# Optimization experiments

Measured on AMD Instinct MI355X. Metric: run time of the kernel, lower is better.

Reference implementation:

```python
import jax, jax.numpy as jnp
import numpy as np

EMBED_DIM = 1024
NUM_HEADS = 16
HEAD_DIM = EMBED_DIM // NUM_HEADS
B, T = 2, 2048


def setup_inputs() -> dict:
    key = jax.random.key(0)
    ks = jax.random.split(key, 9)
    s = 1.0 / np.sqrt(EMBED_DIM)
    x = jax.random.normal(ks[0], (B, T, EMBED_DIM), dtype=jnp.float32)
    Wq = jax.random.uniform(ks[1], (EMBED_DIM, EMBED_DIM), jnp.float32, -s, s)
    bq = jax.random.uniform(ks[2], (EMBED_DIM,), jnp.float32, -s, s)
    Wk = jax.random.uniform(ks[3], (EMBED_DIM, EMBED_DIM), jnp.float32, -s, s)
    bk = jax.random.uniform(ks[4], (EMBED_DIM,), jnp.float32, -s, s)
    Wv = jax.random.uniform(ks[5], (EMBED_DIM, EMBED_DIM), jnp.float32, -s, s)
    bv = jax.random.uniform(ks[6], (EMBED_DIM,), jnp.float32, -s, s)
    Wo = jax.random.uniform(ks[7], (EMBED_DIM, EMBED_DIM), jnp.float32, -s, s)
    bo = jax.random.uniform(ks[8], (EMBED_DIM,), jnp.float32, -s, s)
    return {"x": x, "Wq": Wq, "bq": bq, "Wk": Wk, "bk": bk,
            "Wv": Wv, "bv": bv, "Wo": Wo, "bo": bo}


def reference(x, Wq, bq, Wk, bk, Wv, bv, Wo, bo):
    Bx, Tx, D = x.shape
    # projections (torch Linear: y = x @ W^T + b); here W stored as [in, out]
    q = (x @ Wq + bq).reshape(Bx, Tx, NUM_HEADS, HEAD_DIM).transpose(0, 2, 1, 3)
    k = (x @ Wk + bk).reshape(Bx, Tx, NUM_HEADS, HEAD_DIM).transpose(0, 2, 1, 3)
    v = (x @ Wv + bv).reshape(Bx, Tx, NUM_HEADS, HEAD_DIM).transpose(0, 2, 1, 3)
    scale = HEAD_DIM ** -0.5
    attn = jnp.einsum('bhqd,bhkd->bhqk', q, k) * scale  # [B, H, T, T]
    causal = jnp.tril(jnp.ones((Tx, Tx), dtype=bool))
    attn = jnp.where(causal[None, None], attn, -jnp.inf)
    attn = jax.nn.softmax(attn, axis=-1)
    out = jnp.einsum('bhqk,bhkd->bhqd', attn, v)  # [B, H, T, hd]
    out = out.transpose(0, 2, 1, 3).reshape(Bx, Tx, D)
    return out @ Wo + bo
```

## Files before the change

kernel.cpp:

```cpp
#include <hip/hip_runtime.h>

#define EMBED 1024
#define NHEADS 16
#define HDIM 64
#define SEQ 2048
#define BATCH 2
#define MROWS (BATCH * SEQ)

using bf16x8 = __attribute__((ext_vector_type(8))) short;
using f32x4  = __attribute__((ext_vector_type(4))) float;
using us4    = __attribute__((ext_vector_type(4))) unsigned short;
using u32x2  = __attribute__((ext_vector_type(2))) unsigned int;

__device__ __forceinline__ unsigned short f2bf(float f) {
    unsigned int u = __builtin_bit_cast(unsigned int, f);
    u = (u + 0x7fffu + ((u >> 16) & 1u)) >> 16;
    return (unsigned short)u;
}

__device__ __forceinline__ unsigned int cvt_pk_bf16(float a, float b) {
    unsigned int d;
    asm("v_cvt_pk_bf16_f32 %0, %1, %2" : "=v"(d) : "v"(a), "v"(b));
    return d;
}

__device__ __forceinline__ void async16(const unsigned short* g, unsigned short* l) {
    __builtin_amdgcn_global_load_lds(
        (const __attribute__((address_space(1))) void*)g,
        (__attribute__((address_space(3))) void*)l, 16, 0, 0);
}

__global__ __launch_bounds__(256)
void cvt_all(const float* __restrict__ X, unsigned short* __restrict__ XO,
             const float* __restrict__ W0, const float* __restrict__ W1,
             const float* __restrict__ W2, const float* __restrict__ W3,
             unsigned short* __restrict__ T0, unsigned short* __restrict__ T1,
             unsigned short* __restrict__ T2, unsigned short* __restrict__ T3)
{
    const int tid = threadIdx.x;
    if (blockIdx.z == 4) {
        const int blk = blockIdx.y * 16 + blockIdx.x;
#pragma unroll
        for (int it = 0; it < 16; ++it) {
            int i = (blk * 16 + it) * 256 + tid;
            float4 v = ((const float4*)X)[i];
            us4 o;
            o[0] = f2bf(v.x); o[1] = f2bf(v.y); o[2] = f2bf(v.z); o[3] = f2bf(v.w);
            ((us4*)XO)[i] = o;
        }
        return;
    }
    const float* W = blockIdx.z == 0 ? W0 : blockIdx.z == 1 ? W1 :
                     blockIdx.z == 2 ? W2 : W3;
    unsigned short* T = blockIdx.z == 0 ? T0 : blockIdx.z == 1 ? T1 :
                        blockIdx.z == 2 ? T2 : T3;
    __shared__ unsigned short tile[64][72];
    const int k0 = blockIdx.y << 6, n0 = blockIdx.x << 6;
    const int lr = tid >> 4, lc = (tid & 15) << 2;
#pragma unroll
    for (int it = 0; it < 4; ++it) {
        int kr = lr + it * 16;
        float4 v = *(const float4*)(W + (size_t)(k0 + kr) * EMBED + n0 + lc);
        tile[lc + 0][kr] = f2bf(v.x);
        tile[lc + 1][kr] = f2bf(v.y);
        tile[lc + 2][kr] = f2bf(v.z);
        tile[lc + 3][kr] = f2bf(v.w);
    }
    __syncthreads();
#pragma unroll
    for (int it = 0; it < 4; ++it) {
        int nr = lr + it * 16;
        us4 o = *(const us4*)(&tile[nr][lc]);
        *(us4*)(T + (size_t)(n0 + nr) * EMBED + k0 + lc) = o;
    }
}

__device__ __forceinline__ void mfma_gemm_core(
    const unsigned short* __restrict__ A, const unsigned short* __restrict__ Bt,
    int bm, int n0, unsigned short* As, unsigned short* Bs,
    int wv, int lane, f32x4 acc[4][4])
{
    const int m16 = lane & 15, quad = lane >> 4;
    const int mb = (wv >> 1) << 6;
    const int nb = (wv & 1) << 6;
    const int rsw = m16 & 3;

    const int srow0 = lane >> 2;
    const int gcol  = ((lane & 3) ^ (srow0 & 3)) << 3;
    const unsigned short* ga = A  + (size_t)(bm + wv * 16 + srow0) * EMBED + gcol;
    const unsigned short* gb = Bt + (size_t)(n0 + wv * 16 + srow0) * EMBED + gcol;

    int offA[4], offB[4];
#pragma unroll
    for (int i = 0; i < 4; ++i) {
        offA[i] = (mb + i * 16 + m16) * 32;
        offB[i] = (nb + i * 16 + m16) * 32;
    }

    const int NK = EMBED / 32;
#define STAGE(t) do {                                                        \
        unsigned short* la = As + ((t) & 1) * (128 * 32) + wv * 16 * 32;     \
        unsigned short* lb = Bs + ((t) & 1) * (128 * 32) + wv * 16 * 32;     \
        const unsigned short* gat = ga + (t) * 32;                           \
        const unsigned short* gbt = gb + (t) * 32;                           \
        async16(gat, la);                                                    \
        async16(gat + 64 * EMBED, la + 64 * 32);                             \
        async16(gbt, lb);                                                    \
        async16(gbt + 64 * EMBED, lb + 64 * 32);                             \
    } while (0)

    STAGE(0);
    for (int t = 0; t < NK; ++t) {
        if (t + 1 < NK) {
            STAGE(t + 1);
            asm volatile("s_waitcnt vmcnt(4)" ::: "memory");
        } else {
            asm volatile("s_waitcnt vmcnt(0)" ::: "memory");
        }
        asm volatile("s_barrier" ::: "memory");
        const unsigned short* Ab = As + (t & 1) * (128 * 32);
        const unsigned short* Bb = Bs + (t & 1) * (128 * 32);
        const int sl = ((quad ^ rsw) << 3);
        bf16x8 af[4], bfv[4];
#pragma unroll
        for (int i = 0; i < 4; ++i) {
            af[i]  = *(const bf16x8*)(Ab + offA[i] + sl);
            bfv[i] = *(const bf16x8*)(Bb + offB[i] + sl);
        }
#pragma unroll
        for (int i = 0; i < 4; ++i)
#pragma unroll
            for (int j = 0; j < 4; ++j)
                acc[i][j] = __builtin_amdgcn_mfma_f32_16x16x32_bf16(
                    af[i], bfv[j], acc[i][j], 0, 0, 0);
        asm volatile("s_barrier" ::: "memory");
    }
#undef STAGE
}

__device__ __forceinline__ void mfma_gemm_core64(
    const unsigned short* __restrict__ A, const unsigned short* __restrict__ Bt,
    int bm, int n0, unsigned short* As, unsigned short* Bs,
    int wv, int lane, f32x4 acc[4][2])
{
    const int m16 = lane & 15, quad = lane >> 4;
    const int mb = (wv >> 1) << 6;
    const int nb = (wv & 1) << 5;
    const int rsw = m16 & 7;

    const int gcol = ((lane & 7) ^ ((lane >> 3) & 7)) << 3;
    const unsigned short* ga = A  + (size_t)(bm + wv * 32 + (lane >> 3)) * EMBED + gcol;
    const unsigned short* gb = Bt + (size_t)(n0 + wv * 16 + (lane >> 3)) * EMBED + gcol;

    int offA[4], offB[2];
#pragma unroll
    for (int i = 0; i < 4; ++i) offA[i] = (mb + i * 16 + m16) * 64;
#pragma unroll
    for (int j = 0; j < 2; ++j) offB[j] = (nb + j * 16 + m16) * 64;

    const int NK = EMBED / 64;
#define STAGE64(t) do {                                                      \
        unsigned short* la = As + ((t) & 1) * (128 * 64) + wv * 32 * 64;     \
        unsigned short* lb = Bs + ((t) & 1) * (64 * 64) + wv * 16 * 64;      \
        const unsigned short* gat = ga + (t) * 64;                           \
        const unsigned short* gbt = gb + (t) * 64;                           \
        _Pragma("unroll")                                                    \
        for (int j = 0; j < 4; ++j)                                          \
            async16(gat + j * 8 * EMBED, la + j * 8 * 64);                   \
        _Pragma("unroll")                                                    \
        for (int j = 0; j < 2; ++j)                                          \
            async16(gbt + j * 8 * EMBED, lb + j * 8 * 64);                   \
    } while (0)

    STAGE64(0);
    for (int t = 0; t < NK; ++t) {
        if (t + 1 < NK) {
            STAGE64(t + 1);
            asm volatile("s_waitcnt vmcnt(6)" ::: "memory");
        } else {
            asm volatile("s_waitcnt vmcnt(0)" ::: "memory");
        }
        asm volatile("s_barrier" ::: "memory");
        const unsigned short* Ab = As + (t & 1) * (128 * 64);
        const unsigned short* Bb = Bs + (t & 1) * (64 * 64);
#pragma unroll
        for (int ks = 0; ks < 2; ++ks) {
            const int sl = (((ks << 2) + quad) ^ rsw) << 3;
            bf16x8 af[4], bfv[2];
#pragma unroll
            for (int i = 0; i < 4; ++i)
                af[i] = *(const bf16x8*)(Ab + offA[i] + sl);
#pragma unroll
            for (int j = 0; j < 2; ++j)
                bfv[j] = *(const bf16x8*)(Bb + offB[j] + sl);
#pragma unroll
            for (int i = 0; i < 4; ++i)
#pragma unroll
                for (int j = 0; j < 2; ++j)
                    acc[i][j] = __builtin_amdgcn_mfma_f32_16x16x32_bf16(
                        af[i], bfv[j], acc[i][j], 0, 0, 0);
        }
        asm volatile("s_barrier" ::: "memory");
    }
#undef STAGE64
}

__global__ __launch_bounds__(256)
void qkv_gemm(const unsigned short* __restrict__ xb,
              const unsigned short* __restrict__ Wtq,
              const unsigned short* __restrict__ Wtk,
              const unsigned short* __restrict__ Wtv,
              const float* __restrict__ bq, const float* __restrict__ bk,
              const float* __restrict__ bv,
              unsigned short* __restrict__ Qo, unsigned short* __restrict__ Ko,
              unsigned short* __restrict__ Vto)
{
    __shared__ __align__(16) unsigned short As[2 * 128 * 32];
    __shared__ __align__(16) unsigned short Bs[2 * 128 * 32];
    const int tid = threadIdx.x, wv = tid >> 6, lane = tid & 63;
    const int m16 = lane & 15, quad = lane >> 4;
    const int which = blockIdx.x >> 3;
    const int n0 = (blockIdx.x & 7) << 7;
    const int bm = blockIdx.y << 7;
    const unsigned short* Bt = which == 0 ? Wtq : which == 1 ? Wtk : Wtv;
    const float* bias = which == 0 ? bq : which == 1 ? bk : bv;

    f32x4 acc[4][4];
#pragma unroll
    for (int i = 0; i < 4; ++i)
#pragma unroll
        for (int j = 0; j < 4; ++j) acc[i][j] = (f32x4){0.f, 0.f, 0.f, 0.f};

    mfma_gemm_core(xb, Bt, bm, n0, As, Bs, wv, lane, acc);

    const int mb = (wv >> 1) << 6, nb = (wv & 1) << 6;
    const float qscale = 0.125f * 1.4426950408889634f;
#pragma unroll
    for (int i = 0; i < 4; ++i) {
        const int m0 = bm + mb + i * 16 + quad * 4;
        const int b = m0 >> 11, t0 = m0 & (SEQ - 1);
#pragma unroll
        for (int j = 0; j < 4; ++j) {
            const int n = n0 + nb + j * 16 + m16;
            const int h = n >> 6, d = n & 63;
            const float bval = bias[n];
            if (which == 2) {
                us4 v;
#pragma unroll
                for (int r = 0; r < 4; ++r) v[r] = f2bf(acc[i][j][r] + bval);
                *(us4*)(Vto + ((((size_t)(b * NHEADS + h)) << 6) + d) * SEQ + t0) = v;
            } else {
                const float sc = which == 0 ? qscale : 1.f;
                unsigned short* dst = (which == 0 ? Qo : Ko) +
                    ((((size_t)(b * NHEADS + h)) << 11) + t0) * 64 + d;
#pragma unroll
                for (int r = 0; r < 4; ++r)
                    dst[(size_t)r * 64] = f2bf((acc[i][j][r] + bval) * sc);
            }
        }
    }
}

__global__ __launch_bounds__(256)
void out_gemm(const unsigned short* __restrict__ aob,
              const unsigned short* __restrict__ Wto,
              const float* __restrict__ bo, float* __restrict__ out)
{
    __shared__ __align__(16) unsigned short As[2 * 128 * 64];
    __shared__ __align__(16) unsigned short Bs[2 * 64 * 64];
    const int tid = threadIdx.x, wv = tid >> 6, lane = tid & 63;
    const int m16 = lane & 15, quad = lane >> 4;
    const int n0 = blockIdx.x << 6;
    const int bm = blockIdx.y << 7;

    f32x4 acc[4][2];
#pragma unroll
    for (int i = 0; i < 4; ++i)
#pragma unroll
        for (int j = 0; j < 2; ++j) acc[i][j] = (f32x4){0.f, 0.f, 0.f, 0.f};

    mfma_gemm_core64(aob, Wto, bm, n0, As, Bs, wv, lane, acc);

    const int mb = (wv >> 1) << 6, nb = (wv & 1) << 5;
#pragma unroll
    for (int i = 0; i < 4; ++i) {
        const int m0 = bm + mb + i * 16 + quad * 4;
#pragma unroll
        for (int j = 0; j < 2; ++j) {
            const int n = n0 + nb + j * 16 + m16;
            const float bval = bo[n];
#pragma unroll
            for (int r = 0; r < 4; ++r)
                out[(size_t)(m0 + r) * EMBED + n] = acc[i][j][r] + bval;
        }
    }
}

__global__ __launch_bounds__(256)
void attn_mfma(const unsigned short* __restrict__ Qb,
               const unsigned short* __restrict__ Kb,
               const unsigned short* __restrict__ Vtb,
               unsigned short* __restrict__ Oout)
{
    __shared__ __align__(16) unsigned short Ks[64 * 64];
    __shared__ __align__(16) unsigned short Vt[64 * 64];
    __shared__ __align__(16) unsigned short Ps[4][16 * 64];

    const int tid  = threadIdx.x;
    const int wv   = tid >> 6;
    const int lane = tid & 63;
    const int m16  = lane & 15;
    const int quad = lane >> 4;
    const int bh   = blockIdx.x;
    const int b    = bh >> 4, h = bh & 15;

    const int yr = blockIdx.y & 7, yk = blockIdx.y >> 3;
    const int qt = yk == 0 ? yr : yk == 1 ? 15 - yr : yk == 2 ? 16 + yr : 31 - yr;
    const int q0 = qt << 6;

    const int srow = tid >> 2;
    const int cc   = tid & 3;
    const int swr  = srow & 7;
    const int sx   = m16 & 7;

    bf16x8 rk0, rk1, rv0, rv1;
    auto load_tile = [&](int k0) {
        const int scol = cc << 4;
        const unsigned short* sk = Kb + (((size_t)bh << 11) + k0 + srow) * 64 + scol;
        rk0 = *(const bf16x8*)sk;
        rk1 = *(const bf16x8*)(sk + 8);
        const unsigned short* sv = Vtb + (((size_t)bh << 6) + srow) * SEQ + k0 + scol;
        rv0 = *(const bf16x8*)sv;
        rv1 = *(const bf16x8*)(sv + 8);
    };

    const size_t qoff =
        (((size_t)bh << 11) + q0 + (wv << 4) + m16) * 64 + (quad << 3);
    bf16x8 qa0 = *(const bf16x8*)(Qb + qoff);
    bf16x8 qa1 = *(const bf16x8*)(Qb + qoff + 32);

    f32x4 o[4];
#pragma unroll
    for (int dt = 0; dt < 4; ++dt) o[dt] = (f32x4){0.f, 0.f, 0.f, 0.f};
    float m_ = -1e30f, l_ = 0.f;

    load_tile(0);

    for (int kt = 0; kt <= qt; ++kt) {
        __syncthreads();
        {
            unsigned short* kd = Ks + srow * 64;
            unsigned short* vd = Vt + srow * 64;
            *(bf16x8*)(kd + (((2 * cc) ^ swr) << 3))     = rk0;
            *(bf16x8*)(kd + (((2 * cc + 1) ^ swr) << 3)) = rk1;
            *(bf16x8*)(vd + (((2 * cc) ^ swr) << 3))     = rv0;
            *(bf16x8*)(vd + (((2 * cc + 1) ^ swr) << 3)) = rv1;
        }
        __syncthreads();
        if (kt < qt) load_tile((kt + 1) << 6);

        const bool diag = (kt == qt);

        f32x4 s[4];
#pragma unroll
        for (int g = 0; g < 4; ++g) {
            if (diag && g > wv) {
                s[g] = (f32x4){-1e30f, -1e30f, -1e30f, -1e30f};
                continue;
            }
            const unsigned short* kr = Ks + (g * 16 + m16) * 64;
            bf16x8 kb0 = *(const bf16x8*)(kr + ((quad ^ sx) << 3));
            bf16x8 kb1 = *(const bf16x8*)(kr + (((quad + 4) ^ sx) << 3));
            s[g] = (f32x4){0.f, 0.f, 0.f, 0.f};
            s[g] = __builtin_amdgcn_mfma_f32_16x16x32_bf16(kb0, qa0, s[g], 0, 0, 0);
            s[g] = __builtin_amdgcn_mfma_f32_16x16x32_bf16(kb1, qa1, s[g], 0, 0, 0);
        }
        if (diag) {
#pragma unroll
            for (int r = 0; r < 4; ++r)
                if (quad * 4 + r > m16) s[wv][r] = -1e30f;
        }

        float mx = fmaxf(fmaxf(s[0][0], s[0][1]), fmaxf(s[0][2], s[0][3]));
#pragma unroll
        for (int g = 1; g < 4; ++g)
            mx = fmaxf(mx, fmaxf(fmaxf(s[g][0], s[g][1]), fmaxf(s[g][2], s[g][3])));
        mx = fmaxf(mx, __shfl_xor(mx, 16));
        mx = fmaxf(mx, __shfl_xor(mx, 32));

        if (mx > m_ + 8.f) {
            const float alpha = exp2f(m_ - mx);
            m_ = mx;
            l_ *= alpha;
#pragma unroll
            for (int dt = 0; dt < 4; ++dt) o[dt] *= alpha;
        }

        float sum = 0.f;
        unsigned int pw0[4], pw1[4];
#pragma unroll
        for (int g = 0; g < 4; ++g) {
            float p0 = exp2f(s[g][0] - m_);
            float p1 = exp2f(s[g][1] - m_);
            float p2 = exp2f(s[g][2] - m_);
            float p3 = exp2f(s[g][3] - m_);
            sum += (p0 + p1) + (p2 + p3);
            pw0[g] = cvt_pk_bf16(p0, p1);
            pw1[g] = cvt_pk_bf16(p2, p3);
        }
        sum += __shfl_xor(sum, 16);
        sum += __shfl_xor(sum, 32);
        l_ += sum;

        {
            unsigned short* pd = Ps[wv] + m16 * 64 + ((quad & 1) << 2);
#pragma unroll
            for (int g = 0; g < 4; ++g) {
                u32x2 w; w.x = pw0[g]; w.y = pw1[g];
                *(u32x2*)(pd + (((2 * g + (quad >> 1)) ^ sx) << 3)) = w;
            }
        }

        const unsigned short* pr = Ps[wv] + m16 * 64;
        bf16x8 pa0 = *(const bf16x8*)(pr + ((quad ^ sx) << 3));
        bf16x8 pa1 = *(const bf16x8*)(pr + (((quad + 4) ^ sx) << 3));
        const bool skip_hi = diag && (wv < 2);
#pragma unroll
        for (int dt = 0; dt < 4; ++dt) {
            const unsigned short* vr = Vt + (dt * 16 + m16) * 64;
            bf16x8 vb0 = *(const bf16x8*)(vr + ((quad ^ sx) << 3));
            o[dt] = __builtin_amdgcn_mfma_f32_16x16x32_bf16(vb0, pa0, o[dt], 0, 0, 0);
            if (!skip_hi) {
                bf16x8 vb1 = *(const bf16x8*)(vr + (((quad + 4) ^ sx) << 3));
                o[dt] = __builtin_amdgcn_mfma_f32_16x16x32_bf16(vb1, pa1, o[dt], 0, 0, 0);
            }
        }
    }

    const float inv = 1.f / l_;
    const int t = q0 + (wv << 4) + m16;
    unsigned short* dst =
        Oout + ((size_t)((b << 11) + t) << 10) + (h << 6) + (quad << 2);
#pragma unroll
    for (int dt = 0; dt < 4; ++dt) {
        u32x2 w;
        w.x = cvt_pk_bf16(o[dt][0] * inv, o[dt][1] * inv);
        w.y = cvt_pk_bf16(o[dt][2] * inv, o[dt][3] * inv);
        *(u32x2*)(dst + dt * 16) = w;
    }
}

extern "C" void kernel_launch(void* const* d_in, const int* in_sizes, int n_in,
                              void* d_out, int out_size, void* d_ws, size_t ws_size,
                              hipStream_t stream) {
    const float* x  = (const float*)d_in[0];
    const float* Wq = (const float*)d_in[1];
    const float* bq = (const float*)d_in[2];
    const float* Wk = (const float*)d_in[3];
    const float* bk = (const float*)d_in[4];
    const float* Wv = (const float*)d_in[5];
    const float* bv = (const float*)d_in[6];
    const float* Wo = (const float*)d_in[7];
    const float* bo = (const float*)d_in[8];
    float* out = (float*)d_out;

    const size_t HSZ = (size_t)MROWS * EMBED;
    const size_t WSZ = (size_t)EMBED * EMBED;
    unsigned short* qb  = (unsigned short*)d_ws;
    unsigned short* kb  = qb + HSZ;
    unsigned short* vtb = kb + HSZ;
    unsigned short* aob = vtb + HSZ;
    unsigned short* xb  = aob + HSZ;
    unsigned short* wtq = xb + HSZ;
    unsigned short* wtk = wtq + WSZ;
    unsigned short* wtv = wtk + WSZ;
    unsigned short* wto = wtv + WSZ;

    cvt_all<<<dim3(16, 16, 5), 256, 0, stream>>>(x, xb, Wq, Wk, Wv, Wo,
                                                 wtq, wtk, wtv, wto);

    qkv_gemm<<<dim3(24, 32), 256, 0, stream>>>(xb, wtq, wtk, wtv, bq, bk, bv,
                                               qb, kb, vtb);

    attn_mfma<<<dim3(32, 32), 256, 0, stream>>>(qb, kb, vtb, aob);

    out_gemm<<<dim3(16, 32), 256, 0, stream>>>(aob, wto, bo, out);
}
```

Baseline: 196.9 us.

## Make attention waves independent with direct K/V register loads and paired causal tasks

```diff
diff --git a/kernel.cpp b/kernel.cpp
--- a/kernel.cpp
+++ b/kernel.cpp
@@ -302,8 +302,6 @@
                const unsigned short* __restrict__ Vtb,
                unsigned short* __restrict__ Oout)
 {
-    __shared__ __align__(16) unsigned short Ks[64 * 64];
-    __shared__ __align__(16) unsigned short Vt[64 * 64];
     __shared__ __align__(16) unsigned short Ps[4][16 * 64];
 
     const int tid  = threadIdx.x;
@@ -311,143 +309,156 @@
     const int lane = tid & 63;
     const int m16  = lane & 15;
     const int quad = lane >> 4;
-    const int bh   = blockIdx.x;
-    const int b    = bh >> 4, h = bh & 15;
-
-    const int yr = blockIdx.y & 7, yk = blockIdx.y >> 3;
-    const int qt = yk == 0 ? yr : yk == 1 ? 15 - yr : yk == 2 ? 16 + yr : 31 - yr;
-    const int q0 = qt << 6;
-
-    const int srow = tid >> 2;
-    const int cc   = tid & 3;
-    const int swr  = srow & 7;
     const int sx   = m16 & 7;
 
-    bf16x8 rk0, rk1, rv0, rv1;
-    auto load_tile = [&](int k0) {
-        const int scol = cc << 4;
-        const unsigned short* sk = Kb + (((size_t)bh << 11) + k0 + srow) * 64 + scol;
-        rk0 = *(const bf16x8*)sk;
-        rk1 = *(const bf16x8*)(sk + 8);
-        const unsigned short* sv = Vtb + (((size_t)bh << 6) + srow) * SEQ + k0 + scol;
-        rv0 = *(const bf16x8*)sv;
-        rv1 = *(const bf16x8*)(sv + 8);
-    };
-
-    const size_t qoff =
-        (((size_t)bh << 11) + q0 + (wv << 4) + m16) * 64 + (quad << 3);
-    bf16x8 qa0 = *(const bf16x8*)(Qb + qoff);
-    bf16x8 qa1 = *(const bf16x8*)(Qb + qoff + 32);
-
-    f32x4 o[4];
-#pragma unroll
-    for (int dt = 0; dt < 4; ++dt) o[dt] = (f32x4){0.f, 0.f, 0.f, 0.f};
-    float m_ = -1e30f, l_ = 0.f;
-
-    load_tile(0);
-
-    for (int kt = 0; kt <= qt; ++kt) {
-        __syncthreads();
-        {
-            unsigned short* kd = Ks + srow * 64;
-            unsigned short* vd = Vt + srow * 64;
-            *(bf16x8*)(kd + (((2 * cc) ^ swr) << 3))     = rk0;
-            *(bf16x8*)(kd + (((2 * cc + 1) ^ swr) << 3)) = rk1;
-            *(bf16x8*)(vd + (((2 * cc) ^ swr) << 3))     = rv0;
-            *(bf16x8*)(vd + (((2 * cc + 1) ^ swr) << 3)) = rv1;
-        }
-        __syncthreads();
-        if (kt < qt) load_tile((kt + 1) << 6);
-
-        const bool diag = (kt == qt);
-
-        f32x4 s[4];
-#pragma unroll
-        for (int g = 0; g < 4; ++g) {
-            if (diag && g > wv) {
-                s[g] = (f32x4){-1e30f, -1e30f, -1e30f, -1e30f};
-                continue;
-            }
-            const unsigned short* kr = Ks + (g * 16 + m16) * 64;
-            bf16x8 kb0 = *(const bf16x8*)(kr + ((quad ^ sx) << 3));
-            bf16x8 kb1 = *(const bf16x8*)(kr + (((quad + 4) ^ sx) << 3));
-            s[g] = (f32x4){0.f, 0.f, 0.f, 0.f};
-            s[g] = __builtin_amdgcn_mfma_f32_16x16x32_bf16(kb0, qa0, s[g], 0, 0, 0);
-            s[g] = __builtin_amdgcn_mfma_f32_16x16x32_bf16(kb1, qa1, s[g], 0, 0, 0);
-        }
-        if (diag) {
-#pragma unroll
-            for (int r = 0; r < 4; ++r)
-                if (quad * 4 + r > m16) s[wv][r] = -1e30f;
-        }
-
-        float mx = fmaxf(fmaxf(s[0][0], s[0][1]), fmaxf(s[0][2], s[0][3]));
-#pragma unroll
-        for (int g = 1; g < 4; ++g)
-            mx = fmaxf(mx, fmaxf(fmaxf(s[g][0], s[g][1]), fmaxf(s[g][2], s[g][3])));
-        mx = fmaxf(mx, __shfl_xor(mx, 16));
-        mx = fmaxf(mx, __shfl_xor(mx, 32));
-
-        if (mx > m_ + 8.f) {
-            const float alpha = exp2f(m_ - mx);
-            m_ = mx;
-            l_ *= alpha;
-#pragma unroll
-            for (int dt = 0; dt < 4; ++dt) o[dt] *= alpha;
-        }
-
-        float sum = 0.f;
-        unsigned int pw0[4], pw1[4];
-#pragma unroll
-        for (int g = 0; g < 4; ++g) {
-            float p0 = exp2f(s[g][0] - m_);
-            float p1 = exp2f(s[g][1] - m_);
-            float p2 = exp2f(s[g][2] - m_);
-            float p3 = exp2f(s[g][3] - m_);
-            sum += (p0 + p1) + (p2 + p3);
-            pw0[g] = cvt_pk_bf16(p0, p1);
-            pw1[g] = cvt_pk_bf16(p2, p3);
-        }
-        sum += __shfl_xor(sum, 16);
-        sum += __shfl_xor(sum, 32);
-        l_ += sum;
-
-        {
-            unsigned short* pd = Ps[wv] + m16 * 64 + ((quad & 1) << 2);
+    const int b8    = blockIdx.x;
+    const int sub   = b8 >> 3;
+    const int bh    = (b8 & 7) * 4 + (sub & 3);
+    const int blk16 = sub >> 2;
+    const int widx  = blk16 * 4 + wv;
+    const int b = bh >> 4, h = bh & 15;
+
+    unsigned short* PsW = Ps[wv];
+
+    const unsigned short* kp = Kb  + (((size_t)bh << 11) + m16) * 64 + (quad << 3);
+    const unsigned short* vp = Vtb + (((size_t)bh << 6)  + m16) * SEQ + (quad << 3);
+
+#define LOADK(DK, KI) do {                                                   \
+        const unsigned short* kq = kp + (size_t)(KI) * 4096;                 \
+        _Pragma("unroll")                                                    \
+        for (int g = 0; g < 4; ++g) {                                        \
+            DK[g][0] = *(const bf16x8*)(kq + g * 1024);                      \
+            DK[g][1] = *(const bf16x8*)(kq + g * 1024 + 32);                 \
+        }                                                                    \
+    } while (0)
+
+    for (int task = 0; task < 2; ++task) {
+        const int p  = task == 0 ? (127 - widx) : widx;
+        const int KT = (p >> 2) + 1;
+        const int gd = p & 3;
+        const int q16 = p << 4;
+
+        const size_t qoff =
+            (((size_t)bh << 11) + q16 + m16) * 64 + (quad << 3);
+        bf16x8 qa0 = *(const bf16x8*)(Qb + qoff);
+        bf16x8 qa1 = *(const bf16x8*)(Qb + qoff + 32);
+
+        f32x4 o[4];
+#pragma unroll
+        for (int dt = 0; dt < 4; ++dt) o[dt] = (f32x4){0.f, 0.f, 0.f, 0.f};
+        float m_ = -1e30f, l_ = 0.f;
+
+        bf16x8 kA[4][2], kB[4][2];
+        LOADK(kA, 0);
+
+        auto step = [&](bf16x8 (&KF)[4][2], bf16x8 (&KN)[4][2], int kt) {
+            bf16x8 VF[4][2];
+            {
+                const unsigned short* vq = vp + kt * 64;
+#pragma unroll
+                for (int dt = 0; dt < 4; ++dt) {
+                    VF[dt][0] = *(const bf16x8*)(vq + dt * 16 * SEQ);
+                    VF[dt][1] = *(const bf16x8*)(vq + dt * 16 * SEQ + 32);
+                }
+            }
+            if (kt + 1 < KT) LOADK(KN, kt + 1);
+
+            const bool diag = (kt == KT - 1);
+
+            f32x4 s[4];
 #pragma unroll
             for (int g = 0; g < 4; ++g) {
-                u32x2 w; w.x = pw0[g]; w.y = pw1[g];
-                *(u32x2*)(pd + (((2 * g + (quad >> 1)) ^ sx) << 3)) = w;
-            }
-        }
-
-        const unsigned short* pr = Ps[wv] + m16 * 64;
-        bf16x8 pa0 = *(const bf16x8*)(pr + ((quad ^ sx) << 3));
-        bf16x8 pa1 = *(const bf16x8*)(pr + (((quad + 4) ^ sx) << 3));
-        const bool skip_hi = diag && (wv < 2);
+                s[g] = (f32x4){0.f, 0.f, 0.f, 0.f};
+                s[g] = __builtin_amdgcn_mfma_f32_16x16x32_bf16(
+                    KF[g][0], qa0, s[g], 0, 0, 0);
+                s[g] = __builtin_amdgcn_mfma_f32_16x16x32_bf16(
+                    KF[g][1], qa1, s[g], 0, 0, 0);
+            }
+            if (diag) {
+                const int qloc = (gd << 4) + m16;
+#pragma unroll
+                for (int g = 0; g < 4; ++g)
+#pragma unroll
+                    for (int r = 0; r < 4; ++r)
+                        if (g * 16 + (quad << 2) + r > qloc) s[g][r] = -1e30f;
+            }
+
+            float mx = fmaxf(fmaxf(s[0][0], s[0][1]), fmaxf(s[0][2], s[0][3]));
+#pragma unroll
+            for (int g = 1; g < 4; ++g)
+                mx = fmaxf(mx, fmaxf(fmaxf(s[g][0], s[g][1]),
+                                     fmaxf(s[g][2], s[g][3])));
+            mx = fmaxf(mx, __shfl_xor(mx, 16));
+            mx = fmaxf(mx, __shfl_xor(mx, 32));
+
+            if (mx > m_ + 8.f) {
+                const float alpha = exp2f(m_ - mx);
+                m_ = mx;
+                l_ *= alpha;
+#pragma unroll
+                for (int dt = 0; dt < 4; ++dt) o[dt] *= alpha;
+            }
+
+            float sum = 0.f;
+            unsigned int pw0[4], pw1[4];
+#pragma unroll
+            for (int g = 0; g < 4; ++g) {
+                float p0 = exp2f(s[g][0] - m_);
+                float p1 = exp2f(s[g][1] - m_);
+                float p2 = exp2f(s[g][2] - m_);
+                float p3 = exp2f(s[g][3] - m_);
+                sum += (p0 + p1) + (p2 + p3);
+                pw0[g] = cvt_pk_bf16(p0, p1);
+                pw1[g] = cvt_pk_bf16(p2, p3);
+            }
+            sum += __shfl_xor(sum, 16);
+            sum += __shfl_xor(sum, 32);
+            l_ += sum;
+
+            {
+                unsigned short* pd = PsW + m16 * 64 + ((quad & 1) << 2);
+#pragma unroll
+                for (int g = 0; g < 4; ++g) {
+                    u32x2 w; w.x = pw0[g]; w.y = pw1[g];
+                    *(u32x2*)(pd + (((2 * g + (quad >> 1)) ^ sx) << 3)) = w;
+                }
+            }
+
+            const unsigned short* pr = PsW + m16 * 64;
+            bf16x8 pa0 = *(const bf16x8*)(pr + ((quad ^ sx) << 3));
+            bf16x8 pa1 = *(const bf16x8*)(pr + (((quad + 4) ^ sx) << 3));
+            const bool skip_hi = diag && (gd < 2);
+#pragma unroll
+            for (int dt = 0; dt < 4; ++dt) {
+                o[dt] = __builtin_amdgcn_mfma_f32_16x16x32_bf16(
+                    VF[dt][0], pa0, o[dt], 0, 0, 0);
+                if (!skip_hi)
+                    o[dt] = __builtin_amdgcn_mfma_f32_16x16x32_bf16(
+                        VF[dt][1], pa1, o[dt], 0, 0, 0);
+            }
+        };
+
+        int kt = 0;
+        for (;;) {
+            step(kA, kB, kt);
+            ++kt; if (kt >= KT) break;
+            step(kB, kA, kt);
+            ++kt; if (kt >= KT) break;
+        }
+
+        const float inv = 1.f / l_;
+        const int t = q16 + m16;
+        unsigned short* dst =
+            Oout + ((size_t)((b << 11) + t) << 10) + (h << 6) + (quad << 2);
 #pragma unroll
         for (int dt = 0; dt < 4; ++dt) {
-            const unsigned short* vr = Vt + (dt * 16 + m16) * 64;
-            bf16x8 vb0 = *(const bf16x8*)(vr + ((quad ^ sx) << 3));
-            o[dt] = __builtin_amdgcn_mfma_f32_16x16x32_bf16(vb0, pa0, o[dt], 0, 0, 0);
-            if (!skip_hi) {
-                bf16x8 vb1 = *(const bf16x8*)(vr + (((quad + 4) ^ sx) << 3));
-                o[dt] = __builtin_amdgcn_mfma_f32_16x16x32_bf16(vb1, pa1, o[dt], 0, 0, 0);
-            }
-        }
-    }
-
-    const float inv = 1.f / l_;
-    const int t = q0 + (wv << 4) + m16;
-    unsigned short* dst =
-        Oout + ((size_t)((b << 11) + t) << 10) + (h << 6) + (quad << 2);
-#pragma unroll
-    for (int dt = 0; dt < 4; ++dt) {
-        u32x2 w;
-        w.x = cvt_pk_bf16(o[dt][0] * inv, o[dt][1] * inv);
-        w.y = cvt_pk_bf16(o[dt][2] * inv, o[dt][3] * inv);
-        *(u32x2*)(dst + dt * 16) = w;
-    }
+            u32x2 w;
+            w.x = cvt_pk_bf16(o[dt][0] * inv, o[dt][1] * inv);
+            w.y = cvt_pk_bf16(o[dt][2] * inv, o[dt][3] * inv);
+            *(u32x2*)(dst + dt * 16) = w;
+        }
+    }
+#undef LOADK
 }
 
 extern "C" void kernel_launch(void* const* d_in, const int* in_sizes, int n_in,
@@ -482,7 +493,7 @@
     qkv_gemm<<<dim3(24, 32), 256, 0, stream>>>(xb, wtq, wtk, wtv, bq, bk, bv,
                                                qb, kb, vtb);
 
-    attn_mfma<<<dim3(32, 32), 256, 0, stream>>>(qb, kb, vtb, aob);
+    attn_mfma<<<dim3(512), 256, 0, stream>>>(qb, kb, vtb, aob);
 
     out_gemm<<<dim3(16, 32), 256, 0, stream>>>(aob, wto, bo, out);
 }
```

Result: slower. 267.2 us (+35.7%).

## Split attention blocks into 2-wave 32-row tiles with heavy-first ordering

Applied to the files above, without the earlier changes.

```diff
diff --git a/kernel.cpp b/kernel.cpp
--- a/kernel.cpp
+++ b/kernel.cpp
@@ -296,7 +296,7 @@
     }
 }
 
-__global__ __launch_bounds__(256)
+__global__ __launch_bounds__(128, 4)
 void attn_mfma(const unsigned short* __restrict__ Qb,
                const unsigned short* __restrict__ Kb,
                const unsigned short* __restrict__ Vtb,
@@ -304,38 +304,45 @@
 {
     __shared__ __align__(16) unsigned short Ks[64 * 64];
     __shared__ __align__(16) unsigned short Vt[64 * 64];
-    __shared__ __align__(16) unsigned short Ps[4][16 * 64];
+    __shared__ __align__(16) unsigned short Ps[2][16 * 64];
 
     const int tid  = threadIdx.x;
     const int wv   = tid >> 6;
     const int lane = tid & 63;
     const int m16  = lane & 15;
     const int quad = lane >> 4;
-    const int bh   = blockIdx.x;
-    const int b    = bh >> 4, h = bh & 15;
-
-    const int yr = blockIdx.y & 7, yk = blockIdx.y >> 3;
-    const int qt = yk == 0 ? yr : yk == 1 ? 15 - yr : yk == 2 ? 16 + yr : 31 - yr;
-    const int q0 = qt << 6;
-
-    const int srow = tid >> 2;
-    const int cc   = tid & 3;
+    const int sx   = m16 & 7;
+
+    const int ord = blockIdx.x >> 5;
+    const int bh  = blockIdx.x & 31;
+    const int j   = 63 - ord;
+    const int b = bh >> 4, h = bh & 15;
+
+    const int p   = 2 * j + wv;
+    const int KT  = (j >> 1) + 1;
+    const int gd  = p & 3;
+    const int q16 = p << 4;
+
+    const int srow = tid >> 1;
+    const int half = tid & 1;
     const int swr  = srow & 7;
-    const int sx   = m16 & 7;
-
-    bf16x8 rk0, rk1, rv0, rv1;
+
+    unsigned short* PsW = Ps[wv];
+
+    bf16x8 rk[4], rv[4];
     auto load_tile = [&](int k0) {
-        const int scol = cc << 4;
+        const int scol = half << 5;
         const unsigned short* sk = Kb + (((size_t)bh << 11) + k0 + srow) * 64 + scol;
-        rk0 = *(const bf16x8*)sk;
-        rk1 = *(const bf16x8*)(sk + 8);
         const unsigned short* sv = Vtb + (((size_t)bh << 6) + srow) * SEQ + k0 + scol;
-        rv0 = *(const bf16x8*)sv;
-        rv1 = *(const bf16x8*)(sv + 8);
+#pragma unroll
+        for (int i = 0; i < 4; ++i) {
+            rk[i] = *(const bf16x8*)(sk + i * 8);
+            rv[i] = *(const bf16x8*)(sv + i * 8);
+        }
     };
 
     const size_t qoff =
-        (((size_t)bh << 11) + q0 + (wv << 4) + m16) * 64 + (quad << 3);
+        (((size_t)bh << 11) + q16 + m16) * 64 + (quad << 3);
     bf16x8 qa0 = *(const bf16x8*)(Qb + qoff);
     bf16x8 qa1 = *(const bf16x8*)(Qb + qoff + 32);
 
@@ -346,25 +353,27 @@
 
     load_tile(0);
 
-    for (int kt = 0; kt <= qt; ++kt) {
+    for (int kt = 0; kt < KT; ++kt) {
         __syncthreads();
         {
             unsigned short* kd = Ks + srow * 64;
             unsigned short* vd = Vt + srow * 64;
-            *(bf16x8*)(kd + (((2 * cc) ^ swr) << 3))     = rk0;
-            *(bf16x8*)(kd + (((2 * cc + 1) ^ swr) << 3)) = rk1;
-            *(bf16x8*)(vd + (((2 * cc) ^ swr) << 3))     = rv0;
-            *(bf16x8*)(vd + (((2 * cc + 1) ^ swr) << 3)) = rv1;
+#pragma unroll
+            for (int i = 0; i < 4; ++i) {
+                const int slot = (half << 2) + i;
+                *(bf16x8*)(kd + ((slot ^ swr) << 3)) = rk[i];
+                *(bf16x8*)(vd + ((slot ^ swr) << 3)) = rv[i];
+            }
         }
         __syncthreads();
-        if (kt < qt) load_tile((kt + 1) << 6);
-
-        const bool diag = (kt == qt);
+        if (kt + 1 < KT) load_tile((kt + 1) << 6);
+
+        const bool diag = (kt == KT - 1);
 
         f32x4 s[4];
 #pragma unroll
         for (int g = 0; g < 4; ++g) {
-            if (diag && g > wv) {
+            if (diag && g > gd) {
                 s[g] = (f32x4){-1e30f, -1e30f, -1e30f, -1e30f};
                 continue;
             }
@@ -376,9 +385,10 @@
             s[g] = __builtin_amdgcn_mfma_f32_16x16x32_bf16(kb1, qa1, s[g], 0, 0, 0);
         }
         if (diag) {
+            const int qloc = (gd << 4) + m16;
 #pragma unroll
             for (int r = 0; r < 4; ++r)
-                if (quad * 4 + r > m16) s[wv][r] = -1e30f;
+                if ((gd << 4) + (quad << 2) + r > qloc) s[gd][r] = -1e30f;
         }
 
         float mx = fmaxf(fmaxf(s[0][0], s[0][1]), fmaxf(s[0][2], s[0][3]));
@@ -413,7 +423,7 @@
         l_ += sum;
 
         {
-            unsigned short* pd = Ps[wv] + m16 * 64 + ((quad & 1) << 2);
+            unsigned short* pd = PsW + m16 * 64 + ((quad & 1) << 2);
 #pragma unroll
             for (int g = 0; g < 4; ++g) {
                 u32x2 w; w.x = pw0[g]; w.y = pw1[g];
@@ -421,10 +431,10 @@
             }
         }
 
-        const unsigned short* pr = Ps[wv] + m16 * 64;
+        const unsigned short* pr = PsW + m16 * 64;
         bf16x8 pa0 = *(const bf16x8*)(pr + ((quad ^ sx) << 3));
         bf16x8 pa1 = *(const bf16x8*)(pr + (((quad + 4) ^ sx) << 3));
-        const bool skip_hi = diag && (wv < 2);
+        const bool skip_hi = diag && (gd < 2);
 #pragma unroll
         for (int dt = 0; dt < 4; ++dt) {
             const unsigned short* vr = Vt + (dt * 16 + m16) * 64;
@@ -438,7 +448,7 @@
     }
 
     const float inv = 1.f / l_;
-    const int t = q0 + (wv << 4) + m16;
+    const int t = q16 + m16;
     unsigned short* dst =
         Oout + ((size_t)((b << 11) + t) << 10) + (h << 6) + (quad << 2);
 #pragma unroll
@@ -482,7 +492,7 @@
     qkv_gemm<<<dim3(24, 32), 256, 0, stream>>>(xb, wtq, wtk, wtv, bq, bk, bv,
                                                qb, kb, vtb);
 
-    attn_mfma<<<dim3(32, 32), 256, 0, stream>>>(qb, kb, vtb, aob);
+    attn_mfma<<<dim3(2048), 128, 0, stream>>>(qb, kb, vtb, aob);
 
     out_gemm<<<dim3(16, 32), 256, 0, stream>>>(aob, wto, bo, out);
 }
```

New measurement: 200.4 us. No clear change (+1.8%).
